# Kernel optimization log

Measured on AMD Instinct MI355X. Metric: run time of the kernel, lower is better.

## Reference

```python
import jax, jax.numpy as jnp
import numpy as np

N_QUBITS = 4
N_LAYERS = 2
DIM = 2 ** N_QUBITS  # 16
BATCH, INPUT_SIZE, HIDDEN_SIZE = 65536, 128, 512

# PennyLane default.qubit convention: wire 0 is the most significant bit.
def _cnot_perm(c, t, n=N_QUBITS):
    idx = np.arange(2 ** n)
    cbit = (idx >> (n - 1 - c)) & 1
    return np.where(cbit == 1, idx ^ (1 << (n - 1 - t)), idx)

# ring of CNOTs: control j -> target (j+1)%n
CNOT_PERMS = [jnp.asarray(_cnot_perm(j, (j + 1) % N_QUBITS)) for j in range(N_QUBITS)]
_idx = np.arange(DIM)
Z_SIGNS = jnp.asarray(np.stack([1.0 - 2.0 * ((_idx >> (N_QUBITS - 1 - j)) & 1) for j in range(N_QUBITS)], axis=1).astype(np.float32))  # [16, 4]


def _rx(t):
    c = jnp.cos(t / 2).astype(jnp.complex64)
    s = (-1j * jnp.sin(t / 2)).astype(jnp.complex64)
    return jnp.stack([jnp.stack([c, s]), jnp.stack([s, c])])


def _ry(t):
    c = jnp.cos(t / 2).astype(jnp.complex64)
    s = jnp.sin(t / 2).astype(jnp.complex64)
    return jnp.stack([jnp.stack([c, -s]), jnp.stack([s, c])])


def _rz(t):
    e = jnp.exp(-0.5j * t.astype(jnp.complex64))
    z = jnp.zeros((), jnp.complex64)
    return jnp.stack([jnp.stack([e, z]), jnp.stack([z, jnp.conj(e)])])


def _apply_1q(state, gate, j, n=N_QUBITS):
    # state: [B, 2^n] complex; gate: [2,2] (shared) or [B,2,2] (per-sample)
    B = state.shape[0]
    st = state.reshape(B, 2 ** j, 2, 2 ** (n - 1 - j))
    if gate.ndim == 2:
        st = jnp.einsum('ij,bajc->baic', gate, st)
    else:
        st = jnp.einsum('bij,bajc->baic', gate, st)
    return st.reshape(B, 2 ** n)


def _qlayer(angles, qweights):
    # Batched 4-qubit state-vector sim of the PennyLane circuit.
    # angles: [B, 4] float32 (RY embedding); qweights: [2, 4, 3]
    B = angles.shape[0]
    state = jnp.zeros((B, DIM), jnp.complex64).at[:, 0].set(1.0)
    c = jnp.cos(angles / 2).astype(jnp.complex64)
    s = jnp.sin(angles / 2).astype(jnp.complex64)
    for j in range(N_QUBITS):
        gate = jnp.stack([jnp.stack([c[:, j], -s[:, j]], -1), jnp.stack([s[:, j], c[:, j]], -1)], -2)  # [B,2,2]
        state = _apply_1q(state, gate, j)
    for l in range(N_LAYERS):
        for j in range(N_QUBITS):
            state = state[:, CNOT_PERMS[j]]
        for j in range(N_QUBITS):
            state = _apply_1q(state, _rx(qweights[l, j, 0]), j)
            state = _apply_1q(state, _ry(qweights[l, j, 1]), j)
            state = _apply_1q(state, _rz(qweights[l, j, 2]), j)
    probs = state.real ** 2 + state.imag ** 2  # [B, 16]
    return probs @ Z_SIGNS  # [B, 4] expval(PauliZ_j)


def _gate(combined, pw, pb, qw, lw, lb):
    ang = combined @ pw.T + pb  # [B, 4]
    # torch original runs the circuit on detached numpy and wraps the result in
    # torch.tensor -> no gradient flows through the quantum layer.
    q = jax.lax.stop_gradient(_qlayer(ang, qw))
    return q @ lw.T + lb  # [B, hidden]


GATES = ('forget', 'input', 'output', 'cell')


def setup_inputs() -> dict:
    key = jax.random.key(0)
    ks = jax.random.split(key, 3 + 3 * len(GATES))
    inp = {
        'x': jax.random.normal(ks[0], (BATCH, INPUT_SIZE), jnp.float32),
        'h_prev': jax.random.normal(ks[1], (BATCH, HIDDEN_SIZE), jnp.float32),
        'c_prev': jax.random.normal(ks[2], (BATCH, HIDDEN_SIZE), jnp.float32),
    }
    for i, g in enumerate(GATES):
        k0, k1, k2 = ks[3 + 3 * i], ks[4 + 3 * i], ks[5 + 3 * i]
        inp[g + '_proj_w'] = jax.random.normal(k0, (N_QUBITS, INPUT_SIZE + HIDDEN_SIZE), jnp.float32) * 0.02
        inp[g + '_proj_b'] = jnp.zeros((N_QUBITS,), jnp.float32)
        inp[g + '_qw'] = jax.random.normal(k1, (N_LAYERS, N_QUBITS, 3), jnp.float32) * 0.1
        inp[g + '_lin_w'] = jax.random.normal(k2, (HIDDEN_SIZE, N_QUBITS), jnp.float32) * 0.1
        inp[g + '_lin_b'] = jnp.zeros((HIDDEN_SIZE,), jnp.float32)
    return inp


def reference(x, h_prev, c_prev,
              forget_proj_w, forget_proj_b, forget_qw, forget_lin_w, forget_lin_b,
              input_proj_w, input_proj_b, input_qw, input_lin_w, input_lin_b,
              output_proj_w, output_proj_b, output_qw, output_lin_w, output_lin_b,
              cell_proj_w, cell_proj_b, cell_qw, cell_lin_w, cell_lin_b):
    combined = jnp.concatenate([x, h_prev], axis=1)  # [B, in+hid]
    f = jax.nn.sigmoid(_gate(combined, forget_proj_w, forget_proj_b, forget_qw, forget_lin_w, forget_lin_b))
    i = jax.nn.sigmoid(_gate(combined, input_proj_w, input_proj_b, input_qw, input_lin_w, input_lin_b))
    o = jax.nn.sigmoid(_gate(combined, output_proj_w, output_proj_b, output_qw, output_lin_w, output_lin_b))
    g = jnp.tanh(_gate(combined, cell_proj_w, cell_proj_b, cell_qw, cell_lin_w, cell_lin_b))
    c_next = f * c_prev + i * g
    h_next = o * jnp.tanh(c_next)
    return (h_next, c_next)
```

## Files before the change

kernel.cpp:

```cpp
#include <hip/hip_runtime.h>
#include <math.h>

#define BATCHN 65536
#define INPUTN 128
#define HIDDENN 512
#define CATN 640
#define ROWS_LSTM 32

typedef float f2v __attribute__((ext_vector_type(2)));
typedef float f4v __attribute__((ext_vector_type(4)));
typedef short s8v __attribute__((ext_vector_type(8)));

__device__ __forceinline__ unsigned short f2bf_rne(float f) {
  unsigned u = __float_as_uint(f);
  u += 0x7fffu + ((u >> 16) & 1u);
  return (unsigned short)(u >> 16);
}

__device__ __forceinline__ s8v pack_bf16x8(float4 lo, float4 hi) {
  union { s8v s; unsigned u[4]; } r;
  asm("v_cvt_pk_bf16_f32 %0, %1, %2" : "=v"(r.u[0]) : "v"(lo.x), "v"(lo.y));
  asm("v_cvt_pk_bf16_f32 %0, %1, %2" : "=v"(r.u[1]) : "v"(lo.z), "v"(lo.w));
  asm("v_cvt_pk_bf16_f32 %0, %1, %2" : "=v"(r.u[2]) : "v"(hi.x), "v"(hi.y));
  asm("v_cvt_pk_bf16_f32 %0, %1, %2" : "=v"(r.u[3]) : "v"(hi.z), "v"(hi.w));
  return r.s;
}

__global__ void k_prologue(const float* __restrict__ qwF, const float* __restrict__ qwI,
                           const float* __restrict__ qwO, const float* __restrict__ qwC,
                           const float* __restrict__ pwF, const float* __restrict__ pwI,
                           const float* __restrict__ pwO, const float* __restrict__ pwC,
                           float2* __restrict__ U, unsigned short* __restrict__ Bfrag) {
  const int t = threadIdx.x;
  if (t < 64) {
    int g = t >> 4, col = t & 15;
    const float* qw = (g == 0) ? qwF : (g == 1) ? qwI : (g == 2) ? qwO : qwC;

    float sr[16], si[16];
#pragma unroll
    for (int i = 0; i < 16; i++) { sr[i] = (i == col) ? 1.f : 0.f; si[i] = 0.f; }

#pragma unroll
    for (int l = 0; l < 2; l++) {
#pragma unroll
      for (int j = 0; j < 4; j++) {
        const int bc = 8 >> j;
        const int bt = 8 >> ((j + 1) & 3);
        float tr[16], ti[16];
#pragma unroll
        for (int i = 0; i < 16; i++) {
          int src = (i & bc) ? (i ^ bt) : i;
          tr[i] = sr[src]; ti[i] = si[src];
        }
#pragma unroll
        for (int i = 0; i < 16; i++) { sr[i] = tr[i]; si[i] = ti[i]; }
      }
#pragma unroll
      for (int j = 0; j < 4; j++) {
        const int bit = 8 >> j;
        const float thx = qw[(l * 4 + j) * 3 + 0] * 0.5f;
        const float thy = qw[(l * 4 + j) * 3 + 1] * 0.5f;
        const float thz = qw[(l * 4 + j) * 3 + 2] * 0.5f;
        float c, s;
        c = cosf(thx); s = sinf(thx);
#pragma unroll
        for (int i = 0; i < 16; i++) if (!(i & bit)) {
          const int k2 = i | bit;
          const float ar = sr[i], ai = si[i], br = sr[k2], bi = si[k2];
          sr[i]  = c * ar + s * bi;  si[i]  = c * ai - s * br;
          sr[k2] = c * br + s * ai;  si[k2] = c * bi - s * ar;
        }
        c = cosf(thy); s = sinf(thy);
#pragma unroll
        for (int i = 0; i < 16; i++) if (!(i & bit)) {
          const int k2 = i | bit;
          const float ar = sr[i], ai = si[i], br = sr[k2], bi = si[k2];
          sr[i]  = c * ar - s * br;  si[i]  = c * ai - s * bi;
          sr[k2] = s * ar + c * br;  si[k2] = s * ai + c * bi;
        }
        c = cosf(thz); s = sinf(thz);
#pragma unroll
        for (int i = 0; i < 16; i++) if (!(i & bit)) {
          const int k2 = i | bit;
          const float ar = sr[i], ai = si[i], br = sr[k2], bi = si[k2];
          sr[i]  = c * ar + s * ai;  si[i]  = c * ai - s * ar;
          sr[k2] = c * br - s * bi;  si[k2] = c * bi + s * br;
        }
      }
    }
#pragma unroll
    for (int m = 0; m < 16; m++)
      U[(g * 16 + m) * 16 + col] = make_float2(sr[m], si[m]);
  }

  for (int e = t; e < 20 * 64; e += 256) {
    const int s = e >> 6, l = e & 63;
    const int n = l & 15, kb = l >> 4;
    const int gate = n >> 2, orow = n & 3;
    const float* pw = (gate == 0) ? pwF : (gate == 1) ? pwI : (gate == 2) ? pwO : pwC;
    const int k0 = s * 32 + kb * 8;
    unsigned short* dst = Bfrag + (size_t)e * 8;
#pragma unroll
    for (int j = 0; j < 8; ++j) dst[j] = f2bf_rne(pw[orow * CATN + k0 + j]);
  }
}

__global__ __launch_bounds__(256) void k_proj_q(
    const float* __restrict__ x, const float* __restrict__ hprev,
    const float* __restrict__ pbF, const float* __restrict__ pbI,
    const float* __restrict__ pbO, const float* __restrict__ pbC,
    const float2* __restrict__ U, const unsigned short* __restrict__ Bfrag,
    float* __restrict__ qv) {
  __shared__ float angL[64 * 17];
  const int tid = threadIdx.x;
  const int lane = tid & 63;
  const int wv = tid >> 6;
  const int m0 = wv * 16;
  const size_t rb = (size_t)blockIdx.x * 64;
  const int mr = lane & 15;
  const int kb = lane >> 4;
  const size_t arow = rb + m0 + mr;

  f4v acc = {0.f, 0.f, 0.f, 0.f};

  const float* xr = x + arow * INPUTN + kb * 8;
#pragma unroll
  for (int T = 0; T < 2; ++T) {
    const float4 l0 = *(const float4*)(xr + T * 64);
    const float4 h0 = *(const float4*)(xr + T * 64 + 4);
    const float4 l1 = *(const float4*)(xr + T * 64 + 32);
    const float4 h1 = *(const float4*)(xr + T * 64 + 36);
    const s8v b0 = *(const s8v*)(Bfrag + ((size_t)(T * 2 + 0) * 64 + lane) * 8);
    const s8v b1 = *(const s8v*)(Bfrag + ((size_t)(T * 2 + 1) * 64 + lane) * 8);
    acc = __builtin_amdgcn_mfma_f32_16x16x32_bf16(pack_bf16x8(l0, h0), b0, acc, 0, 0, 0);
    acc = __builtin_amdgcn_mfma_f32_16x16x32_bf16(pack_bf16x8(l1, h1), b1, acc, 0, 0, 0);
  }
  const float* hr = hprev + arow * HIDDENN + kb * 8;
#pragma unroll 2
  for (int T = 0; T < 8; ++T) {
    const float4 l0 = *(const float4*)(hr + T * 64);
    const float4 h0 = *(const float4*)(hr + T * 64 + 4);
    const float4 l1 = *(const float4*)(hr + T * 64 + 32);
    const float4 h1 = *(const float4*)(hr + T * 64 + 36);
    const s8v b0 = *(const s8v*)(Bfrag + ((size_t)((T + 2) * 2 + 0) * 64 + lane) * 8);
    const s8v b1 = *(const s8v*)(Bfrag + ((size_t)((T + 2) * 2 + 1) * 64 + lane) * 8);
    acc = __builtin_amdgcn_mfma_f32_16x16x32_bf16(pack_bf16x8(l0, h0), b0, acc, 0, 0, 0);
    acc = __builtin_amdgcn_mfma_f32_16x16x32_bf16(pack_bf16x8(l1, h1), b1, acc, 0, 0, 0);
  }

#pragma unroll
  for (int r = 0; r < 4; ++r)
    angL[(m0 + (lane >> 4) * 4 + r) * 17 + (lane & 15)] = acc[r];
  __syncthreads();

  const int row = tid & 63;
  const float* pbg = (wv == 0) ? pbF : (wv == 1) ? pbI : (wv == 2) ? pbO : pbC;
  float ang[4];
#pragma unroll
  for (int j = 0; j < 4; ++j) ang[j] = angL[row * 17 + wv * 4 + j] + pbg[j];

  float cs[4], sn[4];
#pragma unroll
  for (int j = 0; j < 4; j++) __sincosf(ang[j] * 0.5f, &sn[j], &cs[j]);
  float psi[16];
#pragma unroll
  for (int c16 = 0; c16 < 16; c16++) {
    float p = ((c16 & 8) ? sn[0] : cs[0]);
    p *= ((c16 & 4) ? sn[1] : cs[1]);
    p *= ((c16 & 2) ? sn[2] : cs[2]);
    p *= ((c16 & 1) ? sn[3] : cs[3]);
    psi[c16] = p;
  }
  const float2* Ug = U + wv * 256;
  float q0 = 0.f, q1 = 0.f, q2 = 0.f, q3 = 0.f;
#pragma unroll
  for (int m = 0; m < 16; m++) {
    float ssr = 0.f, ssi = 0.f;
#pragma unroll
    for (int c16 = 0; c16 < 16; c16++) {
      const float2 u = Ug[m * 16 + c16];
      ssr += u.x * psi[c16];
      ssi += u.y * psi[c16];
    }
    const float p = ssr * ssr + ssi * ssi;
    q0 = (m & 8) ? q0 - p : q0 + p;
    q1 = (m & 4) ? q1 - p : q1 + p;
    q2 = (m & 2) ? q2 - p : q2 + p;
    q3 = (m & 1) ? q3 - p : q3 + p;
  }
  *(float4*)(qv + (rb + row) * 16 + wv * 4) = make_float4(q0, q1, q2, q3);
}

__device__ __forceinline__ float sigmf(float v) {
  return __builtin_amdgcn_rcpf(1.f + __expf(-v));
}
__device__ __forceinline__ float tanhfast(float v) {
  return 1.f - 2.f * __builtin_amdgcn_rcpf(__expf(2.f * v) + 1.f);
}

__global__ __launch_bounds__(256) void k_lstm(
    const float* __restrict__ qv, const float* __restrict__ cprev,
    const float* __restrict__ lwF, const float* __restrict__ lbF,
    const float* __restrict__ lwI, const float* __restrict__ lbI,
    const float* __restrict__ lwO, const float* __restrict__ lbO,
    const float* __restrict__ lwC, const float* __restrict__ lbC,
    float* __restrict__ out) {
  const int tid = threadIdx.x;
  const int h0 = tid * 2;
  const int rb = blockIdx.x * ROWS_LSTM;

  float4 wF[2], wI[2], wO[2], wC[2];
  float bFv[2], bIv[2], bOv[2], bCv[2];
#pragma unroll
  for (int hh = 0; hh < 2; ++hh) {
    const int hp = h0 + hh;
    wF[hh] = *(const float4*)(lwF + (size_t)hp * 4);
    wI[hh] = *(const float4*)(lwI + (size_t)hp * 4);
    wO[hh] = *(const float4*)(lwO + (size_t)hp * 4);
    wC[hh] = *(const float4*)(lwC + (size_t)hp * 4);
    bFv[hh] = lbF[hp]; bIv[hh] = lbI[hp]; bOv[hh] = lbO[hp]; bCv[hh] = lbC[hp];
  }

#pragma unroll 2
  for (int it = 0; it < ROWS_LSTM; ++it) {
    const int r = rb + it;
    const float* q = qv + (size_t)r * 16;
    const float4 qF = *(const float4*)(q);
    const float4 qI = *(const float4*)(q + 4);
    const float4 qO = *(const float4*)(q + 8);
    const float4 qC = *(const float4*)(q + 12);

    const f2v cp = __builtin_nontemporal_load(
        (const f2v*)(cprev + (size_t)r * HIDDENN + h0));
    float hn[2], cn[2];
#pragma unroll
    for (int hh = 0; hh < 2; ++hh) {
      const float pf = bFv[hh] + wF[hh].x * qF.x + wF[hh].y * qF.y + wF[hh].z * qF.z + wF[hh].w * qF.w;
      const float pi = bIv[hh] + wI[hh].x * qI.x + wI[hh].y * qI.y + wI[hh].z * qI.z + wI[hh].w * qI.w;
      const float po = bOv[hh] + wO[hh].x * qO.x + wO[hh].y * qO.y + wO[hh].z * qO.z + wO[hh].w * qO.w;
      const float pg = bCv[hh] + wC[hh].x * qC.x + wC[hh].y * qC.y + wC[hh].z * qC.z + wC[hh].w * qC.w;
      const float f  = sigmf(pf);
      const float ii = sigmf(pi);
      const float oo = sigmf(po);
      const float gg = tanhfast(pg);
      const float cc = f * cp[hh] + ii * gg;
      cn[hh] = cc;
      hn[hh] = oo * tanhfast(cc);
    }
    f2v hv; hv[0] = hn[0]; hv[1] = hn[1];
    f2v cv; cv[0] = cn[0]; cv[1] = cn[1];
    __builtin_nontemporal_store(hv, (f2v*)(out + (size_t)r * HIDDENN + h0));
    __builtin_nontemporal_store(cv,
        (f2v*)(out + (size_t)BATCHN * HIDDENN + (size_t)r * HIDDENN + h0));
  }
}

extern "C" void kernel_launch(void* const* d_in, const int* in_sizes, int n_in,
                              void* d_out, int out_size, void* d_ws, size_t ws_size,
                              hipStream_t stream) {
  const float* x  = (const float*)d_in[0];
  const float* h  = (const float*)d_in[1];
  const float* c  = (const float*)d_in[2];
  const float* pwF = (const float*)d_in[3];
  const float* pbF = (const float*)d_in[4];
  const float* qwF = (const float*)d_in[5];
  const float* lwF = (const float*)d_in[6];
  const float* lbF = (const float*)d_in[7];
  const float* pwI = (const float*)d_in[8];
  const float* pbI = (const float*)d_in[9];
  const float* qwI = (const float*)d_in[10];
  const float* lwI = (const float*)d_in[11];
  const float* lbI = (const float*)d_in[12];
  const float* pwO = (const float*)d_in[13];
  const float* pbO = (const float*)d_in[14];
  const float* qwO = (const float*)d_in[15];
  const float* lwO = (const float*)d_in[16];
  const float* lbO = (const float*)d_in[17];
  const float* pwC = (const float*)d_in[18];
  const float* pbC = (const float*)d_in[19];
  const float* qwC = (const float*)d_in[20];
  const float* lwC = (const float*)d_in[21];
  const float* lbC = (const float*)d_in[22];

  float* ws = (float*)d_ws;
  float* qv = ws;
  float2* U = (float2*)(ws + (size_t)BATCHN * 16);
  unsigned short* Bfrag =
      (unsigned short*)(ws + (size_t)BATCHN * 16 + 2048);

  k_prologue<<<dim3(1), dim3(256), 0, stream>>>(qwF, qwI, qwO, qwC,
                                                pwF, pwI, pwO, pwC, U, Bfrag);
  k_proj_q<<<dim3(BATCHN / 64), dim3(256), 0, stream>>>(x, h, pbF, pbI, pbO, pbC,
                                                        U, Bfrag, qv);
  k_lstm<<<dim3(BATCHN / ROWS_LSTM), dim3(256), 0, stream>>>(qv, c, lwF, lbF, lwI, lbI,
                                                             lwO, lbO, lwC, lbC,
                                                             (float*)d_out);
}
```

Before: 140.2 us.

## Fuse projection/quantum kernel with LSTM epilogue via shared-memory staging

Merges the projection+quantum-circuit kernel and the LSTM elementwise kernel into one launch. Per-row quantum expectations are kept in LDS instead of a global scratch buffer, which removes the qv round trip and one launch. The cost is a longer kernel per block: each block now handles 64 rows of LSTM work with 256 threads, the memory-heavy and compute-heavy phases run back to back inside a block, and occupancy depends on the new launch bound.

```diff
diff --git a/kernel.cpp b/kernel.cpp
--- a/kernel.cpp
+++ b/kernel.cpp
@@ -5,7 +5,6 @@
 #define INPUTN 128
 #define HIDDENN 512
 #define CATN 640
-#define ROWS_LSTM 32
 
 typedef float f2v __attribute__((ext_vector_type(2)));
 typedef float f4v __attribute__((ext_vector_type(4)));
@@ -24,6 +23,13 @@
   asm("v_cvt_pk_bf16_f32 %0, %1, %2" : "=v"(r.u[2]) : "v"(hi.x), "v"(hi.y));
   asm("v_cvt_pk_bf16_f32 %0, %1, %2" : "=v"(r.u[3]) : "v"(hi.z), "v"(hi.w));
   return r.s;
+}
+
+__device__ __forceinline__ float sigmf(float v) {
+  return __builtin_amdgcn_rcpf(1.f + __expf(-v));
+}
+__device__ __forceinline__ float tanhfast(float v) {
+  return 1.f - 2.f * __builtin_amdgcn_rcpf(__expf(2.f * v) + 1.f);
 }
 
 __global__ void k_prologue(const float* __restrict__ qwF, const float* __restrict__ qwI,
@@ -105,153 +111,150 @@
   }
 }
 
-__global__ __launch_bounds__(256) void k_proj_q(
+__global__ __launch_bounds__(256, 4) void k_fused(
     const float* __restrict__ x, const float* __restrict__ hprev,
     const float* __restrict__ pbF, const float* __restrict__ pbI,
     const float* __restrict__ pbO, const float* __restrict__ pbC,
     const float2* __restrict__ U, const unsigned short* __restrict__ Bfrag,
-    float* __restrict__ qv) {
+    const float* __restrict__ cprev,
+    const float* __restrict__ lwF, const float* __restrict__ lbF,
+    const float* __restrict__ lwI, const float* __restrict__ lbI,
+    const float* __restrict__ lwO, const float* __restrict__ lbO,
+    const float* __restrict__ lwC, const float* __restrict__ lbC,
+    float* __restrict__ out) {
   __shared__ float angL[64 * 17];
+  __shared__ float qL[64 * 20];
   const int tid = threadIdx.x;
   const int lane = tid & 63;
   const int wv = tid >> 6;
   const int m0 = wv * 16;
   const size_t rb = (size_t)blockIdx.x * 64;
-  const int mr = lane & 15;
-  const int kb = lane >> 4;
-  const size_t arow = rb + m0 + mr;
-
-  f4v acc = {0.f, 0.f, 0.f, 0.f};
-
-  const float* xr = x + arow * INPUTN + kb * 8;
-#pragma unroll
-  for (int T = 0; T < 2; ++T) {
-    const float4 l0 = *(const float4*)(xr + T * 64);
-    const float4 h0 = *(const float4*)(xr + T * 64 + 4);
-    const float4 l1 = *(const float4*)(xr + T * 64 + 32);
-    const float4 h1 = *(const float4*)(xr + T * 64 + 36);
-    const s8v b0 = *(const s8v*)(Bfrag + ((size_t)(T * 2 + 0) * 64 + lane) * 8);
-    const s8v b1 = *(const s8v*)(Bfrag + ((size_t)(T * 2 + 1) * 64 + lane) * 8);
-    acc = __builtin_amdgcn_mfma_f32_16x16x32_bf16(pack_bf16x8(l0, h0), b0, acc, 0, 0, 0);
-    acc = __builtin_amdgcn_mfma_f32_16x16x32_bf16(pack_bf16x8(l1, h1), b1, acc, 0, 0, 0);
-  }
-  const float* hr = hprev + arow * HIDDENN + kb * 8;
+
+  {
+    const int mr = lane & 15;
+    const int kb = lane >> 4;
+    const size_t arow = rb + m0 + mr;
+
+    f4v acc = {0.f, 0.f, 0.f, 0.f};
+
+    const float* xr = x + arow * INPUTN + kb * 8;
+#pragma unroll
+    for (int T = 0; T < 2; ++T) {
+      const float4 l0 = *(const float4*)(xr + T * 64);
+      const float4 h0 = *(const float4*)(xr + T * 64 + 4);
+      const float4 l1 = *(const float4*)(xr + T * 64 + 32);
+      const float4 h1 = *(const float4*)(xr + T * 64 + 36);
+      const s8v b0 = *(const s8v*)(Bfrag + ((size_t)(T * 2 + 0) * 64 + lane) * 8);
+      const s8v b1 = *(const s8v*)(Bfrag + ((size_t)(T * 2 + 1) * 64 + lane) * 8);
+      acc = __builtin_amdgcn_mfma_f32_16x16x32_bf16(pack_bf16x8(l0, h0), b0, acc, 0, 0, 0);
+      acc = __builtin_amdgcn_mfma_f32_16x16x32_bf16(pack_bf16x8(l1, h1), b1, acc, 0, 0, 0);
+    }
+    const float* hr = hprev + arow * HIDDENN + kb * 8;
 #pragma unroll 2
-  for (int T = 0; T < 8; ++T) {
-    const float4 l0 = *(const float4*)(hr + T * 64);
-    const float4 h0 = *(const float4*)(hr + T * 64 + 4);
-    const float4 l1 = *(const float4*)(hr + T * 64 + 32);
-    const float4 h1 = *(const float4*)(hr + T * 64 + 36);
-    const s8v b0 = *(const s8v*)(Bfrag + ((size_t)((T + 2) * 2 + 0) * 64 + lane) * 8);
-    const s8v b1 = *(const s8v*)(Bfrag + ((size_t)((T + 2) * 2 + 1) * 64 + lane) * 8);
-    acc = __builtin_amdgcn_mfma_f32_16x16x32_bf16(pack_bf16x8(l0, h0), b0, acc, 0, 0, 0);
-    acc = __builtin_amdgcn_mfma_f32_16x16x32_bf16(pack_bf16x8(l1, h1), b1, acc, 0, 0, 0);
-  }
-
-#pragma unroll
-  for (int r = 0; r < 4; ++r)
-    angL[(m0 + (lane >> 4) * 4 + r) * 17 + (lane & 15)] = acc[r];
+    for (int T = 0; T < 8; ++T) {
+      const float4 l0 = *(const float4*)(hr + T * 64);
+      const float4 h0 = *(const float4*)(hr + T * 64 + 4);
+      const float4 l1 = *(const float4*)(hr + T * 64 + 32);
+      const float4 h1 = *(const float4*)(hr + T * 64 + 36);
+      const s8v b0 = *(const s8v*)(Bfrag + ((size_t)((T + 2) * 2 + 0) * 64 + lane) * 8);
+      const s8v b1 = *(const s8v*)(Bfrag + ((size_t)((T + 2) * 2 + 1) * 64 + lane) * 8);
+      acc = __builtin_amdgcn_mfma_f32_16x16x32_bf16(pack_bf16x8(l0, h0), b0, acc, 0, 0, 0);
+      acc = __builtin_amdgcn_mfma_f32_16x16x32_bf16(pack_bf16x8(l1, h1), b1, acc, 0, 0, 0);
+    }
+
+#pragma unroll
+    for (int r = 0; r < 4; ++r)
+      angL[(m0 + (lane >> 4) * 4 + r) * 17 + (lane & 15)] = acc[r];
+  }
   __syncthreads();
 
-  const int row = tid & 63;
-  const float* pbg = (wv == 0) ? pbF : (wv == 1) ? pbI : (wv == 2) ? pbO : pbC;
-  float ang[4];
-#pragma unroll
-  for (int j = 0; j < 4; ++j) ang[j] = angL[row * 17 + wv * 4 + j] + pbg[j];
-
-  float cs[4], sn[4];
-#pragma unroll
-  for (int j = 0; j < 4; j++) __sincosf(ang[j] * 0.5f, &sn[j], &cs[j]);
-  float psi[16];
-#pragma unroll
-  for (int c16 = 0; c16 < 16; c16++) {
-    float p = ((c16 & 8) ? sn[0] : cs[0]);
-    p *= ((c16 & 4) ? sn[1] : cs[1]);
-    p *= ((c16 & 2) ? sn[2] : cs[2]);
-    p *= ((c16 & 1) ? sn[3] : cs[3]);
-    psi[c16] = p;
-  }
-  const float2* Ug = U + wv * 256;
-  float q0 = 0.f, q1 = 0.f, q2 = 0.f, q3 = 0.f;
-#pragma unroll
-  for (int m = 0; m < 16; m++) {
-    float ssr = 0.f, ssi = 0.f;
+  {
+    const int row = tid & 63;
+    const float* pbg = (wv == 0) ? pbF : (wv == 1) ? pbI : (wv == 2) ? pbO : pbC;
+    float ang[4];
+#pragma unroll
+    for (int j = 0; j < 4; ++j) ang[j] = angL[row * 17 + wv * 4 + j] + pbg[j];
+
+    float cs[4], sn[4];
+#pragma unroll
+    for (int j = 0; j < 4; j++) __sincosf(ang[j] * 0.5f, &sn[j], &cs[j]);
+    float psi[16];
 #pragma unroll
     for (int c16 = 0; c16 < 16; c16++) {
-      const float2 u = Ug[m * 16 + c16];
-      ssr += u.x * psi[c16];
-      ssi += u.y * psi[c16];
-    }
-    const float p = ssr * ssr + ssi * ssi;
-    q0 = (m & 8) ? q0 - p : q0 + p;
-    q1 = (m & 4) ? q1 - p : q1 + p;
-    q2 = (m & 2) ? q2 - p : q2 + p;
-    q3 = (m & 1) ? q3 - p : q3 + p;
-  }
-  *(float4*)(qv + (rb + row) * 16 + wv * 4) = make_float4(q0, q1, q2, q3);
-}
-
-__device__ __forceinline__ float sigmf(float v) {
-  return __builtin_amdgcn_rcpf(1.f + __expf(-v));
-}
-__device__ __forceinline__ float tanhfast(float v) {
-  return 1.f - 2.f * __builtin_amdgcn_rcpf(__expf(2.f * v) + 1.f);
-}
-
-__global__ __launch_bounds__(256) void k_lstm(
-    const float* __restrict__ qv, const float* __restrict__ cprev,
-    const float* __restrict__ lwF, const float* __restrict__ lbF,
-    const float* __restrict__ lwI, const float* __restrict__ lbI,
-    const float* __restrict__ lwO, const float* __restrict__ lbO,
-    const float* __restrict__ lwC, const float* __restrict__ lbC,
-    float* __restrict__ out) {
-  const int tid = threadIdx.x;
-  const int h0 = tid * 2;
-  const int rb = blockIdx.x * ROWS_LSTM;
-
-  float4 wF[2], wI[2], wO[2], wC[2];
-  float bFv[2], bIv[2], bOv[2], bCv[2];
-#pragma unroll
-  for (int hh = 0; hh < 2; ++hh) {
-    const int hp = h0 + hh;
-    wF[hh] = *(const float4*)(lwF + (size_t)hp * 4);
-    wI[hh] = *(const float4*)(lwI + (size_t)hp * 4);
-    wO[hh] = *(const float4*)(lwO + (size_t)hp * 4);
-    wC[hh] = *(const float4*)(lwC + (size_t)hp * 4);
-    bFv[hh] = lbF[hp]; bIv[hh] = lbI[hp]; bOv[hh] = lbO[hp]; bCv[hh] = lbC[hp];
-  }
+      float p = ((c16 & 8) ? sn[0] : cs[0]);
+      p *= ((c16 & 4) ? sn[1] : cs[1]);
+      p *= ((c16 & 2) ? sn[2] : cs[2]);
+      p *= ((c16 & 1) ? sn[3] : cs[3]);
+      psi[c16] = p;
+    }
+    const float2* Ug = U + wv * 256;
+    float q0 = 0.f, q1 = 0.f, q2 = 0.f, q3 = 0.f;
+#pragma unroll
+    for (int m = 0; m < 16; m++) {
+      float ssr = 0.f, ssi = 0.f;
+#pragma unroll
+      for (int c16 = 0; c16 < 16; c16++) {
+        const float2 u = Ug[m * 16 + c16];
+        ssr += u.x * psi[c16];
+        ssi += u.y * psi[c16];
+      }
+      const float p = ssr * ssr + ssi * ssi;
+      q0 = (m & 8) ? q0 - p : q0 + p;
+      q1 = (m & 4) ? q1 - p : q1 + p;
+      q2 = (m & 2) ? q2 - p : q2 + p;
+      q3 = (m & 1) ? q3 - p : q3 + p;
+    }
+    *(float4*)&qL[row * 20 + wv * 4] = make_float4(q0, q1, q2, q3);
+  }
+  __syncthreads();
+
+  {
+    const int h0 = tid * 2;
+
+    float4 wF[2], wI[2], wO[2], wC[2];
+    float bFv[2], bIv[2], bOv[2], bCv[2];
+#pragma unroll
+    for (int hh = 0; hh < 2; ++hh) {
+      const int hp = h0 + hh;
+      wF[hh] = *(const float4*)(lwF + (size_t)hp * 4);
+      wI[hh] = *(const float4*)(lwI + (size_t)hp * 4);
+      wO[hh] = *(const float4*)(lwO + (size_t)hp * 4);
+      wC[hh] = *(const float4*)(lwC + (size_t)hp * 4);
+      bFv[hh] = lbF[hp]; bIv[hh] = lbI[hp]; bOv[hh] = lbO[hp]; bCv[hh] = lbC[hp];
+    }
 
 #pragma unroll 2
-  for (int it = 0; it < ROWS_LSTM; ++it) {
-    const int r = rb + it;
-    const float* q = qv + (size_t)r * 16;
-    const float4 qF = *(const float4*)(q);
-    const float4 qI = *(const float4*)(q + 4);
-    const float4 qO = *(const float4*)(q + 8);
-    const float4 qC = *(const float4*)(q + 12);
-
-    const f2v cp = __builtin_nontemporal_load(
-        (const f2v*)(cprev + (size_t)r * HIDDENN + h0));
-    float hn[2], cn[2];
-#pragma unroll
-    for (int hh = 0; hh < 2; ++hh) {
-      const float pf = bFv[hh] + wF[hh].x * qF.x + wF[hh].y * qF.y + wF[hh].z * qF.z + wF[hh].w * qF.w;
-      const float pi = bIv[hh] + wI[hh].x * qI.x + wI[hh].y * qI.y + wI[hh].z * qI.z + wI[hh].w * qI.w;
-      const float po = bOv[hh] + wO[hh].x * qO.x + wO[hh].y * qO.y + wO[hh].z * qO.z + wO[hh].w * qO.w;
-      const float pg = bCv[hh] + wC[hh].x * qC.x + wC[hh].y * qC.y + wC[hh].z * qC.z + wC[hh].w * qC.w;
-      const float f  = sigmf(pf);
-      const float ii = sigmf(pi);
-      const float oo = sigmf(po);
-      const float gg = tanhfast(pg);
-      const float cc = f * cp[hh] + ii * gg;
-      cn[hh] = cc;
-      hn[hh] = oo * tanhfast(cc);
-    }
-    f2v hv; hv[0] = hn[0]; hv[1] = hn[1];
-    f2v cv; cv[0] = cn[0]; cv[1] = cn[1];
-    __builtin_nontemporal_store(hv, (f2v*)(out + (size_t)r * HIDDENN + h0));
-    __builtin_nontemporal_store(cv,
-        (f2v*)(out + (size_t)BATCHN * HIDDENN + (size_t)r * HIDDENN + h0));
+    for (int it = 0; it < 64; ++it) {
+      const size_t r = rb + it;
+      const float* q = &qL[it * 20];
+      const float4 qF = *(const float4*)(q);
+      const float4 qI = *(const float4*)(q + 4);
+      const float4 qO = *(const float4*)(q + 8);
+      const float4 qC = *(const float4*)(q + 12);
+
+      const f2v cp = __builtin_nontemporal_load(
+          (const f2v*)(cprev + r * HIDDENN + h0));
+      float hn[2], cn[2];
+#pragma unroll
+      for (int hh = 0; hh < 2; ++hh) {
+        const float pf = bFv[hh] + wF[hh].x * qF.x + wF[hh].y * qF.y + wF[hh].z * qF.z + wF[hh].w * qF.w;
+        const float pi = bIv[hh] + wI[hh].x * qI.x + wI[hh].y * qI.y + wI[hh].z * qI.z + wI[hh].w * qI.w;
+        const float po = bOv[hh] + wO[hh].x * qO.x + wO[hh].y * qO.y + wO[hh].z * qO.z + wO[hh].w * qO.w;
+        const float pg = bCv[hh] + wC[hh].x * qC.x + wC[hh].y * qC.y + wC[hh].z * qC.z + wC[hh].w * qC.w;
+        const float f  = sigmf(pf);
+        const float ii = sigmf(pi);
+        const float oo = sigmf(po);
+        const float gg = tanhfast(pg);
+        const float cc = f * cp[hh] + ii * gg;
+        cn[hh] = cc;
+        hn[hh] = oo * tanhfast(cc);
+      }
+      f2v hv; hv[0] = hn[0]; hv[1] = hn[1];
+      f2v cv; cv[0] = cn[0]; cv[1] = cn[1];
+      __builtin_nontemporal_store(hv, (f2v*)(out + r * HIDDENN + h0));
+      __builtin_nontemporal_store(cv,
+          (f2v*)(out + (size_t)BATCHN * HIDDENN + r * HIDDENN + h0));
+    }
   }
 }
 
@@ -282,17 +285,12 @@
   const float* lwC = (const float*)d_in[21];
   const float* lbC = (const float*)d_in[22];
 
-  float* ws = (float*)d_ws;
-  float* qv = ws;
-  float2* U = (float2*)(ws + (size_t)BATCHN * 16);
-  unsigned short* Bfrag =
-      (unsigned short*)(ws + (size_t)BATCHN * 16 + 2048);
+  float2* U = (float2*)d_ws;
+  unsigned short* Bfrag = (unsigned short*)((char*)d_ws + 8192);
 
   k_prologue<<<dim3(1), dim3(256), 0, stream>>>(qwF, qwI, qwO, qwC,
                                                 pwF, pwI, pwO, pwC, U, Bfrag);
-  k_proj_q<<<dim3(BATCHN / 64), dim3(256), 0, stream>>>(x, h, pbF, pbI, pbO, pbC,
-                                                        U, Bfrag, qv);
-  k_lstm<<<dim3(BATCHN / ROWS_LSTM), dim3(256), 0, stream>>>(qv, c, lwF, lbF, lwI, lbI,
-                                                             lwO, lbO, lwC, lbC,
-                                                             (float*)d_out);
-}
+  k_fused<<<dim3(BATCHN / 64), dim3(256), 0, stream>>>(
+      x, h, pbF, pbI, pbO, pbC, U, Bfrag, c,
+      lwF, lbF, lwI, lbI, lwO, lbO, lwC, lbC, (float*)d_out);
+}
```

Result: slower. 170.1 us (+21.3%).
